# Optimization experiments

Measured on AMD Instinct MI355X. Metric: run time of the kernel, lower is better.

## Reference

```python
import jax, jax.numpy as jnp
import numpy as np

TEMPERATURE = 0.07
NEG_INF = -1e9


def setup_inputs() -> dict:
    key = jax.random.key(0)
    k1, k2, k3, k4, k5 = jax.random.split(key, 5)
    B, L, H = 64, 256, 64
    query_embs = jax.random.normal(k1, (B, L, H), dtype=jnp.float32)
    key_embs = jax.random.normal(k2, (B, L, H), dtype=jnp.float32)
    labels = jax.random.randint(k3, (B,), 0, 2, dtype=jnp.int64)
    q_mask = jax.random.randint(k4, (B, L), 0, 2, dtype=jnp.int32)
    k_mask = jax.random.randint(k5, (B, L), 0, 2, dtype=jnp.int32)
    return {"query_embs": query_embs, "key_embs": key_embs, "labels": labels,
            "q_mask": q_mask, "k_mask": k_mask}


def reference(query_embs, key_embs, labels, q_mask, k_mask):
    # ColBERT-style late interaction over all B x B pairs.
    # sim: (B_q, B_k, Lq, Lk) token-level dot products.
    sim = jnp.einsum('bqh,ckh->bcqk', query_embs, key_embs)
    # Mask out padded key tokens before the max over key positions.
    sim = jnp.where(k_mask[None, :, None, :].astype(bool), sim, NEG_INF)
    maxsim = jnp.max(sim, axis=-1)                      # (B_q, B_k, Lq)
    qm = q_mask[:, None, :].astype(maxsim.dtype)        # (B_q, 1, Lq)
    scores = jnp.sum(maxsim * qm, axis=-1) / TEMPERATURE  # (B_q, B_k)
    # Cross-entropy on rows with labels==1, target = diagonal index.
    logp = jax.nn.log_softmax(scores, axis=-1)
    B = scores.shape[0]
    diag = logp[jnp.arange(B), jnp.arange(B)]           # (B,)
    w = labels.astype(scores.dtype)
    denom = jnp.maximum(jnp.sum(w), 1.0)
    return -jnp.sum(w * diag) / denom
```

## Files before the change

### kernel.cpp

```cpp
#include <hip/hip_runtime.h>
#include <math.h>

#define PB 64
#define PL 256
#define PH 64
#define TEMP 0.07f
#define NEG_INF_F (-1e9f)

#define KSTRIDE 72

typedef short short8 __attribute__((ext_vector_type(8)));
typedef float f32x4 __attribute__((ext_vector_type(4)));

__device__ __forceinline__ unsigned short f32_to_bf16(float f) {
    unsigned int u = __float_as_uint(f);
    u += 0x7FFFu + ((u >> 16) & 1u);
    return (unsigned short)(u >> 16);
}

__global__ void convert_kernel(const float* __restrict__ Q,
                               const float* __restrict__ K,
                               unsigned short* __restrict__ Qb,
                               unsigned short* __restrict__ Kb) {
    const int t = blockIdx.x * blockDim.x + threadIdx.x;
    const int NV4 = (PB * PL * PH) / 4;
    const float4* src;
    unsigned short* dst;
    int i;
    if (t < NV4) { src = (const float4*)Q; dst = Qb; i = t; }
    else         { src = (const float4*)K; dst = Kb; i = t - NV4; }
    float4 v = src[i];
    ushort4 o;
    o.x = f32_to_bf16(v.x); o.y = f32_to_bf16(v.y);
    o.z = f32_to_bf16(v.z); o.w = f32_to_bf16(v.w);
    *(ushort4*)(dst + (size_t)i * 4) = o;
}

__global__ __launch_bounds__(256)
void colbert_scores_mfma(const unsigned short* __restrict__ Qb,
                         const unsigned short* __restrict__ Kb,
                         const int*   __restrict__ qmask,
                         const int*   __restrict__ kmask,
                         float*       __restrict__ scores) {
    const int c = blockIdx.x;
    const int b = blockIdx.y;
    const int tid  = threadIdx.x;
    const int wave = tid >> 6;
    const int lane = tid & 63;
    const int n    = lane & 15;
    const int g    = (lane >> 4) & 3;

    __shared__ __align__(16) unsigned short Ks[PL * KSTRIDE];
    __shared__ int   kmI[PL];
    __shared__ float qmF[PL];
    __shared__ float red[4];

    kmI[tid] = kmask[c * PL + tid];
    qmF[tid] = (float)qmask[b * PL + tid];

    {
        const unsigned short* Kbase = Kb + ((size_t)c * PL) * PH;
        #pragma unroll
        for (int it = 0; it < (PL * PH) / (256 * 8); ++it) {
            int lin = it * 256 + tid;
            int row = lin >> 3;
            int off = lin & 7;
            ushort4 v0 = *(const ushort4*)(Kbase + (size_t)row * PH + off * 8);
            ushort4 v1 = *(const ushort4*)(Kbase + (size_t)row * PH + off * 8 + 4);
            *(ushort4*)(&Ks[row * KSTRIDE + off * 8])     = v0;
            *(ushort4*)(&Ks[row * KSTRIDE + off * 8 + 4]) = v1;
        }
    }

    const int qw0 = wave * 64;
    short8 afrag[4][2];
    {
        const unsigned short* Qrow = Qb + ((size_t)b * PL) * PH;
        #pragma unroll
        for (int rt = 0; rt < 4; ++rt) {
            const unsigned short* p = Qrow + (size_t)(qw0 + rt * 16 + n) * PH + g * 8;
            afrag[rt][0] = *(const short8*)(p);
            afrag[rt][1] = *(const short8*)(p + 32);
        }
    }

    __syncthreads();

    float maxv[4][4];
    #pragma unroll
    for (int rt = 0; rt < 4; ++rt)
        #pragma unroll
        for (int r = 0; r < 4; ++r) maxv[rt][r] = NEG_INF_F;

    for (int ct = 0; ct < 16; ++ct) {
        const int km = kmI[ct * 16 + n];
        const unsigned short* krow = &Ks[(ct * 16 + n) * KSTRIDE + g * 8];
        short8 b0 = *(const short8*)(krow);
        short8 b1 = *(const short8*)(krow + 32);

        f32x4 acc[4];
        #pragma unroll
        for (int rt = 0; rt < 4; ++rt) acc[rt] = (f32x4){0.f, 0.f, 0.f, 0.f};
        #pragma unroll
        for (int rt = 0; rt < 4; ++rt)
            acc[rt] = __builtin_amdgcn_mfma_f32_16x16x32_bf16(afrag[rt][0], b0, acc[rt], 0, 0, 0);
        #pragma unroll
        for (int rt = 0; rt < 4; ++rt)
            acc[rt] = __builtin_amdgcn_mfma_f32_16x16x32_bf16(afrag[rt][1], b1, acc[rt], 0, 0, 0);

        #pragma unroll
        for (int rt = 0; rt < 4; ++rt)
            #pragma unroll
            for (int r = 0; r < 4; ++r) {
                float s = km ? acc[rt][r] : NEG_INF_F;
                maxv[rt][r] = fmaxf(maxv[rt][r], s);
            }
    }

    #pragma unroll
    for (int rt = 0; rt < 4; ++rt)
        #pragma unroll
        for (int r = 0; r < 4; ++r) {
            float mv = maxv[rt][r];
            mv = fmaxf(mv, __shfl_xor(mv, 1, 16));
            mv = fmaxf(mv, __shfl_xor(mv, 2, 16));
            mv = fmaxf(mv, __shfl_xor(mv, 4, 16));
            mv = fmaxf(mv, __shfl_xor(mv, 8, 16));
            maxv[rt][r] = mv;
        }

    float partial = 0.0f;
    if (n == 0) {
        #pragma unroll
        for (int rt = 0; rt < 4; ++rt)
            #pragma unroll
            for (int r = 0; r < 4; ++r) {
                int row = qw0 + rt * 16 + g * 4 + r;
                partial += maxv[rt][r] * qmF[row];
            }
    }
    partial += __shfl_xor(partial, 16, 64);
    partial += __shfl_xor(partial, 32, 64);
    if (lane == 0) red[wave] = partial;
    __syncthreads();
    if (tid == 0) {
        float total = red[0] + red[1] + red[2] + red[3];
        scores[b * PB + c] = total * (1.0f / TEMP);
    }
}

__global__ void finalize_kernel(const float* __restrict__ scores,
                                const int*   __restrict__ labels,
                                float*       __restrict__ out) {
    const int r = threadIdx.x;
    const float* row = scores + r * PB;
    float mx = NEG_INF_F;
    for (int j = 0; j < PB; ++j) mx = fmaxf(mx, row[j]);
    float se = 0.0f;
    for (int j = 0; j < PB; ++j) se += expf(row[j] - mx);
    float logp_diag = row[r] - mx - logf(se);
    float w = (float)labels[r];
    float wd = w * logp_diag;
    #pragma unroll
    for (int off = 32; off >= 1; off >>= 1) {
        wd += __shfl_xor(wd, off, 64);
        w  += __shfl_xor(w,  off, 64);
    }
    if (r == 0) out[0] = -wd / fmaxf(w, 1.0f);
}

extern "C" void kernel_launch(void* const* d_in, const int* in_sizes, int n_in,
                              void* d_out, int out_size, void* d_ws, size_t ws_size,
                              hipStream_t stream) {
    const float* Q      = (const float*)d_in[0];
    const float* K      = (const float*)d_in[1];
    const int*   labels = (const int*)d_in[2];
    const int*   qmask  = (const int*)d_in[3];
    const int*   kmask  = (const int*)d_in[4];
    float*       out    = (float*)d_out;

    char* ws = (char*)d_ws;
    float*          scores = (float*)ws;
    unsigned short* Qb     = (unsigned short*)(ws + 16 * 1024);
    unsigned short* Kb     = (unsigned short*)(ws + 16 * 1024 + 2 * 1024 * 1024);

    const int total_v4 = 2 * (PB * PL * PH) / 4;
    convert_kernel<<<total_v4 / 256, 256, 0, stream>>>(Q, K, Qb, Kb);

    dim3 grid(PB, PB);
    colbert_scores_mfma<<<grid, 256, 0, stream>>>(Qb, Kb, qmask, kmask, scores);
    finalize_kernel<<<1, 64, 0, stream>>>(scores, labels, out);
}
```

Measured before the change: 114.4 us.

## Fuse bf16 conversion into scoring kernel and fold key mask into MFMA bias

Removes the separate fp32-to-bf16 conversion kernel and its workspace round-trip. The scoring kernel now reads fp32 Q and K directly and converts them on the fly with packed bf16 intrinsics. The key mask becomes an additive bias (0 or -1e9) used as the initial MFMA accumulator, which removes the per-element select. The column-tile loop is fully unrolled, and launch bounds request 4 blocks per CU. In exchange, each block now reads twice as many bytes of fp32 K and Q from global memory and repeats the conversion work, since 64 blocks share each K and Q tile.

Result: slower. 125.8 us (+10.0%).

```diff
diff --git a/kernel.cpp b/kernel.cpp
--- a/kernel.cpp
+++ b/kernel.cpp
@@ -1,4 +1,5 @@
 #include <hip/hip_runtime.h>
+#include <hip/hip_bf16.h>
 #include <math.h>
 
 #define PB 64
@@ -12,33 +13,16 @@
 typedef short short8 __attribute__((ext_vector_type(8)));
 typedef float f32x4 __attribute__((ext_vector_type(4)));
 
-__device__ __forceinline__ unsigned short f32_to_bf16(float f) {
-    unsigned int u = __float_as_uint(f);
-    u += 0x7FFFu + ((u >> 16) & 1u);
-    return (unsigned short)(u >> 16);
+__device__ __forceinline__ unsigned int pkbf(float a, float b) {
+    __hip_bfloat162 h = __float22bfloat162_rn(float2{a, b});
+    union { __hip_bfloat162 h2; unsigned int u; } cvt;
+    cvt.h2 = h;
+    return cvt.u;
 }
 
-__global__ void convert_kernel(const float* __restrict__ Q,
-                               const float* __restrict__ K,
-                               unsigned short* __restrict__ Qb,
-                               unsigned short* __restrict__ Kb) {
-    const int t = blockIdx.x * blockDim.x + threadIdx.x;
-    const int NV4 = (PB * PL * PH) / 4;
-    const float4* src;
-    unsigned short* dst;
-    int i;
-    if (t < NV4) { src = (const float4*)Q; dst = Qb; i = t; }
-    else         { src = (const float4*)K; dst = Kb; i = t - NV4; }
-    float4 v = src[i];
-    ushort4 o;
-    o.x = f32_to_bf16(v.x); o.y = f32_to_bf16(v.y);
-    o.z = f32_to_bf16(v.z); o.w = f32_to_bf16(v.w);
-    *(ushort4*)(dst + (size_t)i * 4) = o;
-}
-
-__global__ __launch_bounds__(256)
-void colbert_scores_mfma(const unsigned short* __restrict__ Qb,
-                         const unsigned short* __restrict__ Kb,
+__global__ __launch_bounds__(256, 4)
+void colbert_scores_mfma(const float* __restrict__ Qg,
+                         const float* __restrict__ Kg,
                          const int*   __restrict__ qmask,
                          const int*   __restrict__ kmask,
                          float*       __restrict__ scores) {
@@ -51,40 +35,54 @@
     const int g    = (lane >> 4) & 3;
 
     __shared__ __align__(16) unsigned short Ks[PL * KSTRIDE];
-    __shared__ int   kmI[PL];
+    __shared__ float bmF[PL];
     __shared__ float qmF[PL];
     __shared__ float red[4];
 
-    kmI[tid] = kmask[c * PL + tid];
+    bmF[tid] = kmask[c * PL + tid] ? 0.0f : NEG_INF_F;
     qmF[tid] = (float)qmask[b * PL + tid];
 
     {
-        const unsigned short* Kbase = Kb + ((size_t)c * PL) * PH;
+        const float* Kbase = Kg + ((size_t)c * PL) * PH;
         #pragma unroll
-        for (int it = 0; it < (PL * PH) / (256 * 8); ++it) {
+        for (int it = 0; it < (PL * PH) / (256 * 4); ++it) {
             int lin = it * 256 + tid;
-            int row = lin >> 3;
-            int off = lin & 7;
-            ushort4 v0 = *(const ushort4*)(Kbase + (size_t)row * PH + off * 8);
-            ushort4 v1 = *(const ushort4*)(Kbase + (size_t)row * PH + off * 8 + 4);
-            *(ushort4*)(&Ks[row * KSTRIDE + off * 8])     = v0;
-            *(ushort4*)(&Ks[row * KSTRIDE + off * 8 + 4]) = v1;
+            int row = lin >> 4;
+            int c4  = lin & 15;
+            float4 v = *(const float4*)(Kbase + (size_t)lin * 4);
+            uint2 o;
+            o.x = pkbf(v.x, v.y);
+            o.y = pkbf(v.z, v.w);
+            *(uint2*)(&Ks[row * KSTRIDE + c4 * 4]) = o;
         }
     }
 
     const int qw0 = wave * 64;
     short8 afrag[4][2];
     {
-        const unsigned short* Qrow = Qb + ((size_t)b * PL) * PH;
+        const float* Qrow = Qg + ((size_t)b * PL) * PH;
         #pragma unroll
         for (int rt = 0; rt < 4; ++rt) {
-            const unsigned short* p = Qrow + (size_t)(qw0 + rt * 16 + n) * PH + g * 8;
-            afrag[rt][0] = *(const short8*)(p);
-            afrag[rt][1] = *(const short8*)(p + 32);
+            const float* p = Qrow + (size_t)(qw0 + rt * 16 + n) * PH + g * 8;
+            float4 f0 = *(const float4*)(p);
+            float4 f1 = *(const float4*)(p + 4);
+            float4 f2 = *(const float4*)(p + 32);
+            float4 f3 = *(const float4*)(p + 36);
+            union { short8 s8; unsigned int u[4]; } a0, a1;
+            a0.u[0] = pkbf(f0.x, f0.y); a0.u[1] = pkbf(f0.z, f0.w);
+            a0.u[2] = pkbf(f1.x, f1.y); a0.u[3] = pkbf(f1.z, f1.w);
+            a1.u[0] = pkbf(f2.x, f2.y); a1.u[1] = pkbf(f2.z, f2.w);
+            a1.u[2] = pkbf(f3.x, f3.y); a1.u[3] = pkbf(f3.z, f3.w);
+            afrag[rt][0] = a0.s8;
+            afrag[rt][1] = a1.s8;
         }
     }
 
     __syncthreads();
+
+    float biasv[16];
+    #pragma unroll
+    for (int ct = 0; ct < 16; ++ct) biasv[ct] = bmF[ct * 16 + n];
 
     float maxv[4][4];
     #pragma unroll
@@ -92,18 +90,18 @@
         #pragma unroll
         for (int r = 0; r < 4; ++r) maxv[rt][r] = NEG_INF_F;
 
+    const unsigned short* krow0 = &Ks[n * KSTRIDE + g * 8];
+    #pragma unroll
     for (int ct = 0; ct < 16; ++ct) {
-        const int km = kmI[ct * 16 + n];
-        const unsigned short* krow = &Ks[(ct * 16 + n) * KSTRIDE + g * 8];
-        short8 b0 = *(const short8*)(krow);
-        short8 b1 = *(const short8*)(krow + 32);
+        short8 b0 = *(const short8*)(krow0 + ct * 16 * KSTRIDE);
+        short8 b1 = *(const short8*)(krow0 + ct * 16 * KSTRIDE + 32);
+        const float bias = biasv[ct];
+        const f32x4 bias4 = {bias, bias, bias, bias};
 
         f32x4 acc[4];
         #pragma unroll
-        for (int rt = 0; rt < 4; ++rt) acc[rt] = (f32x4){0.f, 0.f, 0.f, 0.f};
-        #pragma unroll
         for (int rt = 0; rt < 4; ++rt)
-            acc[rt] = __builtin_amdgcn_mfma_f32_16x16x32_bf16(afrag[rt][0], b0, acc[rt], 0, 0, 0);
+            acc[rt] = __builtin_amdgcn_mfma_f32_16x16x32_bf16(afrag[rt][0], b0, bias4, 0, 0, 0);
         #pragma unroll
         for (int rt = 0; rt < 4; ++rt)
             acc[rt] = __builtin_amdgcn_mfma_f32_16x16x32_bf16(afrag[rt][1], b1, acc[rt], 0, 0, 0);
@@ -111,10 +109,8 @@
         #pragma unroll
         for (int rt = 0; rt < 4; ++rt)
             #pragma unroll
-            for (int r = 0; r < 4; ++r) {
-                float s = km ? acc[rt][r] : NEG_INF_F;
-                maxv[rt][r] = fmaxf(maxv[rt][r], s);
-            }
+            for (int r = 0; r < 4; ++r)
+                maxv[rt][r] = fmaxf(maxv[rt][r], acc[rt][r]);
     }
 
     #pragma unroll
@@ -178,16 +174,9 @@
     const int*   qmask  = (const int*)d_in[3];
     const int*   kmask  = (const int*)d_in[4];
     float*       out    = (float*)d_out;
-
-    char* ws = (char*)d_ws;
-    float*          scores = (float*)ws;
-    unsigned short* Qb     = (unsigned short*)(ws + 16 * 1024);
-    unsigned short* Kb     = (unsigned short*)(ws + 16 * 1024 + 2 * 1024 * 1024);
-
-    const int total_v4 = 2 * (PB * PL * PH) / 4;
-    convert_kernel<<<total_v4 / 256, 256, 0, stream>>>(Q, K, Qb, Kb);
+    float*       scores = (float*)d_ws;
 
     dim3 grid(PB, PB);
-    colbert_scores_mfma<<<grid, 256, 0, stream>>>(Qb, Kb, qmask, kmask, scores);
+    colbert_scores_mfma<<<grid, 256, 0, stream>>>(Q, K, qmask, kmask, scores);
     finalize_kernel<<<1, 64, 0, stream>>>(scores, labels, out);
 }
```

## Reuse staged key tile across four query batches per block with atomic score accumulation

Applied to the files above, without the earlier changes.

Each block now stages one key batch in LDS and processes four query batches against it, which cuts redundant K loads and the number of blocks. The key mask is folded into the MFMA accumulator initialisation as an additive bias, and per-wave partial scores go to global memory through atomicAdd instead of an LDS reduction with a barrier. The convert kernel zeroes the scores buffer, and finalize loads each row as float4. The atomic accumulation makes the float summation order nondeterministic. The bias trick also adds -1e9 to real dot products rather than replacing them, which differs slightly from the reference.

New measurement: 243.8 us. 2.13x slower.

```diff
diff --git a/kernel.cpp b/kernel.cpp
--- a/kernel.cpp
+++ b/kernel.cpp
@@ -1,4 +1,5 @@
 #include <hip/hip_runtime.h>
+#include <hip/hip_bf16.h>
 #include <math.h>
 
 #define PB 64
@@ -7,21 +8,24 @@
 #define TEMP 0.07f
 #define NEG_INF_F (-1e9f)
 
+#define BG 4
 #define KSTRIDE 72
 
 typedef short short8 __attribute__((ext_vector_type(8)));
 typedef float f32x4 __attribute__((ext_vector_type(4)));
 
-__device__ __forceinline__ unsigned short f32_to_bf16(float f) {
-    unsigned int u = __float_as_uint(f);
-    u += 0x7FFFu + ((u >> 16) & 1u);
-    return (unsigned short)(u >> 16);
+__device__ __forceinline__ unsigned int pkbf(float a, float b) {
+    __hip_bfloat162 h = __float22bfloat162_rn(float2{a, b});
+    union { __hip_bfloat162 h2; unsigned int u; } cvt;
+    cvt.h2 = h;
+    return cvt.u;
 }
 
 __global__ void convert_kernel(const float* __restrict__ Q,
                                const float* __restrict__ K,
                                unsigned short* __restrict__ Qb,
-                               unsigned short* __restrict__ Kb) {
+                               unsigned short* __restrict__ Kb,
+                               float* __restrict__ scores) {
     const int t = blockIdx.x * blockDim.x + threadIdx.x;
     const int NV4 = (PB * PL * PH) / 4;
     const float4* src;
@@ -30,20 +34,27 @@
     if (t < NV4) { src = (const float4*)Q; dst = Qb; i = t; }
     else         { src = (const float4*)K; dst = Kb; i = t - NV4; }
     float4 v = src[i];
-    ushort4 o;
-    o.x = f32_to_bf16(v.x); o.y = f32_to_bf16(v.y);
-    o.z = f32_to_bf16(v.z); o.w = f32_to_bf16(v.w);
-    *(ushort4*)(dst + (size_t)i * 4) = o;
-}
-
-__global__ __launch_bounds__(256)
+    uint2 o;
+    o.x = pkbf(v.x, v.y);
+    o.y = pkbf(v.z, v.w);
+    *(uint2*)(dst + (size_t)i * 4) = o;
+    if (blockIdx.x == 0) {
+        float4 z = {0.f, 0.f, 0.f, 0.f};
+        float4* s4 = (float4*)scores;
+        #pragma unroll
+        for (int j = 0; j < 4; ++j)
+            s4[threadIdx.x * 4 + j] = z;
+    }
+}
+
+__global__ __launch_bounds__(256, 4)
 void colbert_scores_mfma(const unsigned short* __restrict__ Qb,
                          const unsigned short* __restrict__ Kb,
                          const int*   __restrict__ qmask,
                          const int*   __restrict__ kmask,
                          float*       __restrict__ scores) {
-    const int c = blockIdx.x;
-    const int b = blockIdx.y;
+    const int c  = blockIdx.x;
+    const int b0 = blockIdx.y * BG;
     const int tid  = threadIdx.x;
     const int wave = tid >> 6;
     const int lane = tid & 63;
@@ -51,101 +62,135 @@
     const int g    = (lane >> 4) & 3;
 
     __shared__ __align__(16) unsigned short Ks[PL * KSTRIDE];
-    __shared__ int   kmI[PL];
-    __shared__ float qmF[PL];
-    __shared__ float red[4];
-
-    kmI[tid] = kmask[c * PL + tid];
-    qmF[tid] = (float)qmask[b * PL + tid];
 
     {
-        const unsigned short* Kbase = Kb + ((size_t)c * PL) * PH;
-        #pragma unroll
-        for (int it = 0; it < (PL * PH) / (256 * 8); ++it) {
+        const unsigned short* Kbase = Kb + (size_t)c * PL * PH;
+        #pragma unroll
+        for (int it = 0; it < 8; ++it) {
             int lin = it * 256 + tid;
             int row = lin >> 3;
             int off = lin & 7;
-            ushort4 v0 = *(const ushort4*)(Kbase + (size_t)row * PH + off * 8);
-            ushort4 v1 = *(const ushort4*)(Kbase + (size_t)row * PH + off * 8 + 4);
-            *(ushort4*)(&Ks[row * KSTRIDE + off * 8])     = v0;
-            *(ushort4*)(&Ks[row * KSTRIDE + off * 8 + 4]) = v1;
-        }
-    }
+            short8 v = *(const short8*)(Kbase + (size_t)row * PH + off * 8);
+            *(short8*)(&Ks[row * KSTRIDE + off * 8]) = v;
+        }
+    }
+
+    float biasv[16];
+    #pragma unroll
+    for (int ct = 0; ct < 16; ++ct)
+        biasv[ct] = kmask[c * PL + ct * 16 + n] ? 0.0f : NEG_INF_F;
+
+    __syncthreads();
 
     const int qw0 = wave * 64;
-    short8 afrag[4][2];
+
+    float pmax[4][4];
+    int prev_b = -1;
+
+    for (int ib = 0; ib < BG; ++ib) {
+        const int b = b0 + ib;
+
+        short8 afrag[4][2];
+        {
+            const unsigned short* Qrow = Qb + (size_t)b * PL * PH;
+            #pragma unroll
+            for (int rt = 0; rt < 4; ++rt) {
+                const unsigned short* p = Qrow + (size_t)(qw0 + rt * 16 + n) * PH + g * 8;
+                afrag[rt][0] = *(const short8*)(p);
+                afrag[rt][1] = *(const short8*)(p + 32);
+            }
+        }
+
+        if (prev_b >= 0) {
+            #pragma unroll
+            for (int rt = 0; rt < 4; ++rt)
+                #pragma unroll
+                for (int r = 0; r < 4; ++r) {
+                    float m = pmax[rt][r];
+                    m = fmaxf(m, __shfl_xor(m, 1, 16));
+                    m = fmaxf(m, __shfl_xor(m, 2, 16));
+                    m = fmaxf(m, __shfl_xor(m, 4, 16));
+                    m = fmaxf(m, __shfl_xor(m, 8, 16));
+                    pmax[rt][r] = m;
+                }
+            float partial = 0.0f;
+            if (n == 0) {
+                #pragma unroll
+                for (int rt = 0; rt < 4; ++rt)
+                    #pragma unroll
+                    for (int r = 0; r < 4; ++r) {
+                        int row = qw0 + rt * 16 + g * 4 + r;
+                        partial += pmax[rt][r] * (float)qmask[prev_b * PL + row];
+                    }
+            }
+            partial += __shfl_xor(partial, 16, 64);
+            partial += __shfl_xor(partial, 32, 64);
+            if (lane == 0)
+                atomicAdd(&scores[prev_b * PB + c], partial * (1.0f / TEMP));
+        }
+
+        float maxv[4][4];
+        #pragma unroll
+        for (int rt = 0; rt < 4; ++rt)
+            #pragma unroll
+            for (int r = 0; r < 4; ++r) maxv[rt][r] = NEG_INF_F;
+
+        const unsigned short* krow0 = &Ks[n * KSTRIDE + g * 8];
+        #pragma unroll
+        for (int ct = 0; ct < 16; ++ct) {
+            short8 kb0 = *(const short8*)(krow0 + ct * 16 * KSTRIDE);
+            short8 kb1 = *(const short8*)(krow0 + ct * 16 * KSTRIDE + 32);
+            const float bias = biasv[ct];
+            const f32x4 bias4 = {bias, bias, bias, bias};
+
+            f32x4 acc[4];
+            #pragma unroll
+            for (int rt = 0; rt < 4; ++rt)
+                acc[rt] = __builtin_amdgcn_mfma_f32_16x16x32_bf16(afrag[rt][0], kb0, bias4, 0, 0, 0);
+            #pragma unroll
+            for (int rt = 0; rt < 4; ++rt)
+                acc[rt] = __builtin_amdgcn_mfma_f32_16x16x32_bf16(afrag[rt][1], kb1, acc[rt], 0, 0, 0);
+
+            #pragma unroll
+            for (int rt = 0; rt < 4; ++rt)
+                #pragma unroll
+                for (int r = 0; r < 4; ++r)
+                    maxv[rt][r] = fmaxf(maxv[rt][r], acc[rt][r]);
+        }
+
+        #pragma unroll
+        for (int rt = 0; rt < 4; ++rt)
+            #pragma unroll
+            for (int r = 0; r < 4; ++r) pmax[rt][r] = maxv[rt][r];
+        prev_b = b;
+    }
+
     {
-        const unsigned short* Qrow = Qb + ((size_t)b * PL) * PH;
-        #pragma unroll
-        for (int rt = 0; rt < 4; ++rt) {
-            const unsigned short* p = Qrow + (size_t)(qw0 + rt * 16 + n) * PH + g * 8;
-            afrag[rt][0] = *(const short8*)(p);
-            afrag[rt][1] = *(const short8*)(p + 32);
-        }
-    }
-
-    __syncthreads();
-
-    float maxv[4][4];
-    #pragma unroll
-    for (int rt = 0; rt < 4; ++rt)
-        #pragma unroll
-        for (int r = 0; r < 4; ++r) maxv[rt][r] = NEG_INF_F;
-
-    for (int ct = 0; ct < 16; ++ct) {
-        const int km = kmI[ct * 16 + n];
-        const unsigned short* krow = &Ks[(ct * 16 + n) * KSTRIDE + g * 8];
-        short8 b0 = *(const short8*)(krow);
-        short8 b1 = *(const short8*)(krow + 32);
-
-        f32x4 acc[4];
-        #pragma unroll
-        for (int rt = 0; rt < 4; ++rt) acc[rt] = (f32x4){0.f, 0.f, 0.f, 0.f};
         #pragma unroll
         for (int rt = 0; rt < 4; ++rt)
-            acc[rt] = __builtin_amdgcn_mfma_f32_16x16x32_bf16(afrag[rt][0], b0, acc[rt], 0, 0, 0);
-        #pragma unroll
-        for (int rt = 0; rt < 4; ++rt)
-            acc[rt] = __builtin_amdgcn_mfma_f32_16x16x32_bf16(afrag[rt][1], b1, acc[rt], 0, 0, 0);
-
-        #pragma unroll
-        for (int rt = 0; rt < 4; ++rt)
             #pragma unroll
             for (int r = 0; r < 4; ++r) {
-                float s = km ? acc[rt][r] : NEG_INF_F;
-                maxv[rt][r] = fmaxf(maxv[rt][r], s);
+                float m = pmax[rt][r];
+                m = fmaxf(m, __shfl_xor(m, 1, 16));
+                m = fmaxf(m, __shfl_xor(m, 2, 16));
+                m = fmaxf(m, __shfl_xor(m, 4, 16));
+                m = fmaxf(m, __shfl_xor(m, 8, 16));
+                pmax[rt][r] = m;
             }
-    }
-
-    #pragma unroll
-    for (int rt = 0; rt < 4; ++rt)
-        #pragma unroll
-        for (int r = 0; r < 4; ++r) {
-            float mv = maxv[rt][r];
-            mv = fmaxf(mv, __shfl_xor(mv, 1, 16));
-            mv = fmaxf(mv, __shfl_xor(mv, 2, 16));
-            mv = fmaxf(mv, __shfl_xor(mv, 4, 16));
-            mv = fmaxf(mv, __shfl_xor(mv, 8, 16));
-            maxv[rt][r] = mv;
-        }
-
-    float partial = 0.0f;
-    if (n == 0) {
-        #pragma unroll
-        for (int rt = 0; rt < 4; ++rt)
-            #pragma unroll
-            for (int r = 0; r < 4; ++r) {
-                int row = qw0 + rt * 16 + g * 4 + r;
-                partial += maxv[rt][r] * qmF[row];
-            }
-    }
-    partial += __shfl_xor(partial, 16, 64);
-    partial += __shfl_xor(partial, 32, 64);
-    if (lane == 0) red[wave] = partial;
-    __syncthreads();
-    if (tid == 0) {
-        float total = red[0] + red[1] + red[2] + red[3];
-        scores[b * PB + c] = total * (1.0f / TEMP);
+        float partial = 0.0f;
+        if (n == 0) {
+            #pragma unroll
+            for (int rt = 0; rt < 4; ++rt)
+                #pragma unroll
+                for (int r = 0; r < 4; ++r) {
+                    int row = qw0 + rt * 16 + g * 4 + r;
+                    partial += pmax[rt][r] * (float)qmask[prev_b * PL + row];
+                }
+        }
+        partial += __shfl_xor(partial, 16, 64);
+        partial += __shfl_xor(partial, 32, 64);
+        if (lane == 0)
+            atomicAdd(&scores[prev_b * PB + c], partial * (1.0f / TEMP));
     }
 }
 
@@ -153,12 +198,23 @@
                                 const int*   __restrict__ labels,
                                 float*       __restrict__ out) {
     const int r = threadIdx.x;
-    const float* row = scores + r * PB;
+    float4 v[16];
+    const float4* row4 = (const float4*)(scores + r * PB);
+    #pragma unroll
+    for (int i = 0; i < 16; ++i) v[i] = row4[i];
     float mx = NEG_INF_F;
-    for (int j = 0; j < PB; ++j) mx = fmaxf(mx, row[j]);
+    #pragma unroll
+    for (int i = 0; i < 16; ++i) {
+        mx = fmaxf(mx, fmaxf(fmaxf(v[i].x, v[i].y), fmaxf(v[i].z, v[i].w)));
+    }
     float se = 0.0f;
-    for (int j = 0; j < PB; ++j) se += expf(row[j] - mx);
-    float logp_diag = row[r] - mx - logf(se);
+    #pragma unroll
+    for (int i = 0; i < 16; ++i) {
+        se += expf(v[i].x - mx) + expf(v[i].y - mx) +
+              expf(v[i].z - mx) + expf(v[i].w - mx);
+    }
+    float diag = ((const float*)v)[r & 63];
+    float logp_diag = diag - mx - logf(se);
     float w = (float)labels[r];
     float wd = w * logp_diag;
     #pragma unroll
@@ -185,9 +241,9 @@
     unsigned short* Kb     = (unsigned short*)(ws + 16 * 1024 + 2 * 1024 * 1024);
 
     const int total_v4 = 2 * (PB * PL * PH) / 4;
-    convert_kernel<<<total_v4 / 256, 256, 0, stream>>>(Q, K, Qb, Kb);
-
-    dim3 grid(PB, PB);
+    convert_kernel<<<total_v4 / 256, 256, 0, stream>>>(Q, K, Qb, Kb, scores);
+
+    dim3 grid(PB, PB / BG);
     colbert_scores_mfma<<<grid, 256, 0, stream>>>(Qb, Kb, qmask, kmask, scores);
     finalize_kernel<<<1, 64, 0, stream>>>(scores, labels, out);
 }
```

## Split waves into 2x2 row/column tiles and fold key mask into MFMA bias

Applied to the files above, without the earlier changes.

The score kernel now splits work across waves 2x2. Each wave handles 128 query rows against 8 key tiles, so every loaded key fragment feeds 8 MFMAs instead of 4. The key mask becomes an additive bias that seeds the MFMA accumulator, which removes the per-element select. Row max and sum reductions use DPP, and a shared-memory step combines partial maxima from the two column halves. Smaller changes are packed bf16 conversion, wider 16-byte LDS staging, a launch-bounds occupancy hint and vectorized loads in the finalize kernel, at the cost of more registers per thread and an extra barrier.

Measured after the change: 257.3 us. 125% more time.

```diff
diff --git a/kernel.cpp b/kernel.cpp
--- a/kernel.cpp
+++ b/kernel.cpp
@@ -1,4 +1,5 @@
 #include <hip/hip_runtime.h>
+#include <hip/hip_bf16.h>
 #include <math.h>
 
 #define PB 64
@@ -12,10 +13,37 @@
 typedef short short8 __attribute__((ext_vector_type(8)));
 typedef float f32x4 __attribute__((ext_vector_type(4)));
 
-__device__ __forceinline__ unsigned short f32_to_bf16(float f) {
-    unsigned int u = __float_as_uint(f);
-    u += 0x7FFFu + ((u >> 16) & 1u);
-    return (unsigned short)(u >> 16);
+__device__ __forceinline__ unsigned int pkbf(float a, float b) {
+    __hip_bfloat162 h = __float22bfloat162_rn(float2{a, b});
+    union { __hip_bfloat162 h2; unsigned int u; } cvt;
+    cvt.h2 = h;
+    return cvt.u;
+}
+
+__device__ __forceinline__ float rowmax16(float v) {
+    int x;
+    x = __builtin_amdgcn_update_dpp(0, __float_as_int(v), 0x121, 0xf, 0xf, true);
+    v = fmaxf(v, __int_as_float(x));
+    x = __builtin_amdgcn_update_dpp(0, __float_as_int(v), 0x122, 0xf, 0xf, true);
+    v = fmaxf(v, __int_as_float(x));
+    x = __builtin_amdgcn_update_dpp(0, __float_as_int(v), 0x124, 0xf, 0xf, true);
+    v = fmaxf(v, __int_as_float(x));
+    x = __builtin_amdgcn_update_dpp(0, __float_as_int(v), 0x128, 0xf, 0xf, true);
+    v = fmaxf(v, __int_as_float(x));
+    return v;
+}
+
+__device__ __forceinline__ float rowsum16(float v) {
+    int x;
+    x = __builtin_amdgcn_update_dpp(0, __float_as_int(v), 0x121, 0xf, 0xf, true);
+    v += __int_as_float(x);
+    x = __builtin_amdgcn_update_dpp(0, __float_as_int(v), 0x122, 0xf, 0xf, true);
+    v += __int_as_float(x);
+    x = __builtin_amdgcn_update_dpp(0, __float_as_int(v), 0x124, 0xf, 0xf, true);
+    v += __int_as_float(x);
+    x = __builtin_amdgcn_update_dpp(0, __float_as_int(v), 0x128, 0xf, 0xf, true);
+    v += __int_as_float(x);
+    return v;
 }
 
 __global__ void convert_kernel(const float* __restrict__ Q,
@@ -30,13 +58,13 @@
     if (t < NV4) { src = (const float4*)Q; dst = Qb; i = t; }
     else         { src = (const float4*)K; dst = Kb; i = t - NV4; }
     float4 v = src[i];
-    ushort4 o;
-    o.x = f32_to_bf16(v.x); o.y = f32_to_bf16(v.y);
-    o.z = f32_to_bf16(v.z); o.w = f32_to_bf16(v.w);
-    *(ushort4*)(dst + (size_t)i * 4) = o;
-}
-
-__global__ __launch_bounds__(256)
+    uint2 o;
+    o.x = pkbf(v.x, v.y);
+    o.y = pkbf(v.z, v.w);
+    *(uint2*)(dst + (size_t)i * 4) = o;
+}
+
+__global__ __launch_bounds__(256, 3)
 void colbert_scores_mfma(const unsigned short* __restrict__ Qb,
                          const unsigned short* __restrict__ Kb,
                          const int*   __restrict__ qmask,
@@ -51,34 +79,39 @@
     const int g    = (lane >> 4) & 3;
 
     __shared__ __align__(16) unsigned short Ks[PL * KSTRIDE];
-    __shared__ int   kmI[PL];
     __shared__ float qmF[PL];
-    __shared__ float red[4];
-
-    kmI[tid] = kmask[c * PL + tid];
+    __shared__ __align__(16) float redbuf[2][PL];
+    __shared__ float red4[4];
+
     qmF[tid] = (float)qmask[b * PL + tid];
 
     {
-        const unsigned short* Kbase = Kb + ((size_t)c * PL) * PH;
-        #pragma unroll
-        for (int it = 0; it < (PL * PH) / (256 * 8); ++it) {
+        const unsigned short* Kbase = Kb + (size_t)c * PL * PH;
+        #pragma unroll
+        for (int it = 0; it < 8; ++it) {
             int lin = it * 256 + tid;
             int row = lin >> 3;
             int off = lin & 7;
-            ushort4 v0 = *(const ushort4*)(Kbase + (size_t)row * PH + off * 8);
-            ushort4 v1 = *(const ushort4*)(Kbase + (size_t)row * PH + off * 8 + 4);
-            *(ushort4*)(&Ks[row * KSTRIDE + off * 8])     = v0;
-            *(ushort4*)(&Ks[row * KSTRIDE + off * 8 + 4]) = v1;
+            short8 v = *(const short8*)(Kbase + (size_t)row * PH + off * 8);
+            *(short8*)(&Ks[row * KSTRIDE + off * 8]) = v;
         }
     }
 
-    const int qw0 = wave * 64;
-    short8 afrag[4][2];
+    const int rowbase = (wave & 1) * 128;
+    const int ctbase  = (wave >> 1) * 8;
+    const int pair    = wave >> 1;
+
+    float biasv[8];
+    #pragma unroll
+    for (int j = 0; j < 8; ++j)
+        biasv[j] = kmask[c * PL + (ctbase + j) * 16 + n] ? 0.0f : NEG_INF_F;
+
+    short8 afrag[8][2];
     {
-        const unsigned short* Qrow = Qb + ((size_t)b * PL) * PH;
-        #pragma unroll
-        for (int rt = 0; rt < 4; ++rt) {
-            const unsigned short* p = Qrow + (size_t)(qw0 + rt * 16 + n) * PH + g * 8;
+        const unsigned short* Qrow = Qb + (size_t)b * PL * PH;
+        #pragma unroll
+        for (int rt = 0; rt < 8; ++rt) {
+            const unsigned short* p = Qrow + (size_t)(rowbase + rt * 16 + n) * PH + g * 8;
             afrag[rt][0] = *(const short8*)(p);
             afrag[rt][1] = *(const short8*)(p + 32);
         }
@@ -86,79 +119,81 @@
 
     __syncthreads();
 
-    float maxv[4][4];
-    #pragma unroll
-    for (int rt = 0; rt < 4; ++rt)
+    float maxv[8][4];
+    #pragma unroll
+    for (int rt = 0; rt < 8; ++rt)
         #pragma unroll
         for (int r = 0; r < 4; ++r) maxv[rt][r] = NEG_INF_F;
 
-    for (int ct = 0; ct < 16; ++ct) {
-        const int km = kmI[ct * 16 + n];
-        const unsigned short* krow = &Ks[(ct * 16 + n) * KSTRIDE + g * 8];
-        short8 b0 = *(const short8*)(krow);
-        short8 b1 = *(const short8*)(krow + 32);
-
-        f32x4 acc[4];
-        #pragma unroll
-        for (int rt = 0; rt < 4; ++rt) acc[rt] = (f32x4){0.f, 0.f, 0.f, 0.f};
-        #pragma unroll
-        for (int rt = 0; rt < 4; ++rt)
-            acc[rt] = __builtin_amdgcn_mfma_f32_16x16x32_bf16(afrag[rt][0], b0, acc[rt], 0, 0, 0);
-        #pragma unroll
-        for (int rt = 0; rt < 4; ++rt)
-            acc[rt] = __builtin_amdgcn_mfma_f32_16x16x32_bf16(afrag[rt][1], b1, acc[rt], 0, 0, 0);
-
-        #pragma unroll
-        for (int rt = 0; rt < 4; ++rt)
+    const unsigned short* krow0 = &Ks[n * KSTRIDE + g * 8];
+    #pragma unroll
+    for (int j = 0; j < 8; ++j) {
+        const int ct = ctbase + j;
+        short8 kb0 = *(const short8*)(krow0 + ct * 16 * KSTRIDE);
+        short8 kb1 = *(const short8*)(krow0 + ct * 16 * KSTRIDE + 32);
+        const float bias = biasv[j];
+        const f32x4 bias4 = {bias, bias, bias, bias};
+
+        f32x4 acc[8];
+        #pragma unroll
+        for (int rt = 0; rt < 8; ++rt)
+            acc[rt] = __builtin_amdgcn_mfma_f32_16x16x32_bf16(afrag[rt][0], kb0, bias4, 0, 0, 0);
+        #pragma unroll
+        for (int rt = 0; rt < 8; ++rt)
+            acc[rt] = __builtin_amdgcn_mfma_f32_16x16x32_bf16(afrag[rt][1], kb1, acc[rt], 0, 0, 0);
+
+        #pragma unroll
+        for (int rt = 0; rt < 8; ++rt)
             #pragma unroll
-            for (int r = 0; r < 4; ++r) {
-                float s = km ? acc[rt][r] : NEG_INF_F;
-                maxv[rt][r] = fmaxf(maxv[rt][r], s);
-            }
-    }
-
-    #pragma unroll
-    for (int rt = 0; rt < 4; ++rt)
-        #pragma unroll
-        for (int r = 0; r < 4; ++r) {
-            float mv = maxv[rt][r];
-            mv = fmaxf(mv, __shfl_xor(mv, 1, 16));
-            mv = fmaxf(mv, __shfl_xor(mv, 2, 16));
-            mv = fmaxf(mv, __shfl_xor(mv, 4, 16));
-            mv = fmaxf(mv, __shfl_xor(mv, 8, 16));
-            maxv[rt][r] = mv;
-        }
-
-    float partial = 0.0f;
-    if (n == 0) {
-        #pragma unroll
-        for (int rt = 0; rt < 4; ++rt)
-            #pragma unroll
-            for (int r = 0; r < 4; ++r) {
-                int row = qw0 + rt * 16 + g * 4 + r;
-                partial += maxv[rt][r] * qmF[row];
-            }
-    }
-    partial += __shfl_xor(partial, 16, 64);
-    partial += __shfl_xor(partial, 32, 64);
-    if (lane == 0) red[wave] = partial;
+            for (int r = 0; r < 4; ++r)
+                maxv[rt][r] = fmaxf(maxv[rt][r], acc[rt][r]);
+    }
+
+    #pragma unroll
+    for (int rt = 0; rt < 8; ++rt) {
+        f32x4 m4;
+        m4[0] = rowmax16(maxv[rt][0]);
+        m4[1] = rowmax16(maxv[rt][1]);
+        m4[2] = rowmax16(maxv[rt][2]);
+        m4[3] = rowmax16(maxv[rt][3]);
+        if (n == 0)
+            *(f32x4*)(&redbuf[pair][rowbase + rt * 16 + g * 4]) = m4;
+    }
+
     __syncthreads();
-    if (tid == 0) {
-        float total = red[0] + red[1] + red[2] + red[3];
-        scores[b * PB + c] = total * (1.0f / TEMP);
-    }
+
+    {
+        float m = fmaxf(redbuf[0][tid], redbuf[1][tid]);
+        float val = m * qmF[tid];
+        float s = rowsum16(val);
+        s += __shfl_xor(s, 16, 64);
+        s += __shfl_xor(s, 32, 64);
+        if (lane == 0) red4[wave] = s;
+    }
+    __syncthreads();
+    if (tid == 0)
+        scores[b * PB + c] = (red4[0] + red4[1] + red4[2] + red4[3]) * (1.0f / TEMP);
 }
 
 __global__ void finalize_kernel(const float* __restrict__ scores,
                                 const int*   __restrict__ labels,
                                 float*       __restrict__ out) {
     const int r = threadIdx.x;
-    const float* row = scores + r * PB;
+    float4 v[16];
+    const float4* row4 = (const float4*)(scores + r * PB);
+    #pragma unroll
+    for (int i = 0; i < 16; ++i) v[i] = row4[i];
     float mx = NEG_INF_F;
-    for (int j = 0; j < PB; ++j) mx = fmaxf(mx, row[j]);
+    #pragma unroll
+    for (int i = 0; i < 16; ++i)
+        mx = fmaxf(mx, fmaxf(fmaxf(v[i].x, v[i].y), fmaxf(v[i].z, v[i].w)));
     float se = 0.0f;
-    for (int j = 0; j < PB; ++j) se += expf(row[j] - mx);
-    float logp_diag = row[r] - mx - logf(se);
+    #pragma unroll
+    for (int i = 0; i < 16; ++i)
+        se += expf(v[i].x - mx) + expf(v[i].y - mx) +
+              expf(v[i].z - mx) + expf(v[i].w - mx);
+    float diag = ((const float*)v)[r & 63];
+    float logp_diag = diag - mx - logf(se);
     float w = (float)labels[r];
     float wd = w * logp_diag;
     #pragma unroll
```
